# Optimization experiments

Hardware: AMD Instinct MI355X
Metric: run time of the kernel (lower is better)

The kernel has to match this reference:

```python
import jax, jax.numpy as jnp
import numpy as np

N_NODES = 100000
N_EDGES = 600000
HIDDEN = 128
LN_EPS = 1e-8


def setup_inputs() -> dict:
    key = jax.random.key(0)
    k1, k2, k3 = jax.random.split(key, 3)
    x = jax.random.normal(k1, (N_NODES, HIDDEN), dtype=jnp.float32)
    edge_index = jax.random.randint(k2, (2, N_EDGES), 0, N_NODES, dtype=jnp.int32)
    # GCNConv linear weight (glorot-ish scale) and bias
    W = jax.random.normal(k3, (HIDDEN, HIDDEN), dtype=jnp.float32) / np.sqrt(HIDDEN)
    b = jnp.zeros((HIDDEN,), dtype=jnp.float32)
    ln_gamma = jnp.ones((HIDDEN,), dtype=jnp.float32)
    ln_beta = jnp.zeros((HIDDEN,), dtype=jnp.float32)
    return {"x": x, "edge_index": edge_index, "W": W, "b": b,
            "ln_gamma": ln_gamma, "ln_beta": ln_beta}


def _gcn_layer(x, edge_index, W, b, ln_gamma, ln_beta):
    n = x.shape[0]
    # --- GCNConv (PyG semantics): add self-loops, sym-normalize, x@W, scatter ---
    loop = jnp.arange(n, dtype=edge_index.dtype)
    src = jnp.concatenate([edge_index[0], loop])  # [E+N]
    dst = jnp.concatenate([edge_index[1], loop])
    deg = jax.ops.segment_sum(jnp.ones_like(dst, dtype=x.dtype), dst,
                              num_segments=n)  # in-degree incl. self-loop
    dinv = jnp.where(deg > 0, jax.lax.rsqrt(deg), 0.0)
    norm = dinv[src] * dinv[dst]  # [E+N]
    h = x @ W  # [N, H]
    msg = h[src] * norm[:, None]  # gather + scale, [E+N, H]
    agg = jax.ops.segment_sum(msg, dst, num_segments=n) + b  # scatter-sum
    # --- ReLU -> (dropout = identity in eval) -> residual -> LayerNorm ---
    y = jax.nn.relu(agg) + x
    mu = jnp.mean(y, axis=-1, keepdims=True)
    var = jnp.mean(jnp.square(y - mu), axis=-1, keepdims=True)
    return (y - mu) * jax.lax.rsqrt(var + LN_EPS) * ln_gamma + ln_beta


def reference(x, edge_index, W, b, ln_gamma, ln_beta):
    return _gcn_layer(x, edge_index, W, b, ln_gamma, ln_beta)
```

## Files before the change

### kernel.cpp

```cpp
#include <hip/hip_runtime.h>

#define HID 128
#define CAP 32

typedef unsigned short u16;
typedef unsigned int u32;
typedef __attribute__((ext_vector_type(8))) short short8v;
typedef __attribute__((ext_vector_type(4))) float f32x4;
typedef __attribute__((ext_vector_type(4))) u32 u32x4;

__device__ inline u16 f2bf(float f) {
    union { float f; u32 u; } c; c.f = f;
    u32 u = c.u;
    return (u16)((u + 0x7FFFu + ((u >> 16) & 1u)) >> 16);
}
__device__ inline u32 pack2(float lo, float hi) {
    return (u32)f2bf(lo) | ((u32)f2bf(hi) << 16);
}
__device__ inline float bflo(u32 u) {
    union { u32 u; float f; } c; c.u = u << 16; return c.f;
}
__device__ inline float bfhi(u32 u) {
    union { u32 u; float f; } c; c.u = u & 0xFFFF0000u; return c.f;
}

__global__ void k_countfill(const int* __restrict__ src, const int* __restrict__ dst,
                            int* __restrict__ cnt, int* __restrict__ csr, int e) {
    int i = blockIdx.x * blockDim.x + threadIdx.x;
    if (i < e) {
        int d = dst[i];
        int slot = atomicAdd(&cnt[d], 1);
        if (slot < CAP) csr[(size_t)d * CAP + slot] = src[i];
    }
}

__global__ void k_prep(const int* __restrict__ cnt, float* __restrict__ dinv,
                       const float* __restrict__ W, u16* __restrict__ wswz, int n) {
    int t = blockIdx.x * blockDim.x + threadIdx.x;
    if (t < n) dinv[t] = rsqrtf((float)(cnt[t] + 1));
    if (t < 128 * 128) {
        int i = t & 7;
        int lane = (t >> 3) & 63;
        int ct = (t >> 9) & 7;
        int ks = t >> 12;
        int k = ks * 32 + (lane >> 4) * 8 + i;
        int col = ct * 16 + (lane & 15);
        wswz[t] = f2bf(W[k * HID + col]);
    }
}

__global__ __launch_bounds__(256) void k_gemm(const float* __restrict__ x,
                                              const u16* __restrict__ wswz,
                                              u16* __restrict__ hbf, int n) {
    __shared__ uint4 lds4[2048];
    char* lds = (char*)lds4;
    const int tid = threadIdx.x;
    const int row0 = blockIdx.x * 128;

    #pragma unroll
    for (int it = 0; it < 8; ++it) {
        int c = it * 256 + tid;
        int row = c >> 4;
        int c8 = (c & 15) * 8;
        uint4 payload;
        int gr = row0 + row;
        if (gr < n) {
            const float4* p = (const float4*)&x[(size_t)gr * HID + c8];
            float4 v0 = p[0], v1 = p[1];
            payload.x = pack2(v0.x, v0.y);
            payload.y = pack2(v0.z, v0.w);
            payload.z = pack2(v1.x, v1.y);
            payload.w = pack2(v1.z, v1.w);
        } else {
            payload = make_uint4(0, 0, 0, 0);
        }
        int byte = row * 256 + (c & 15) * 16;
        byte ^= (row & 7) << 4;
        *(uint4*)(lds + byte) = payload;
    }
    __syncthreads();

    const int w = tid >> 6;
    const int l = tid & 63;
    const short8v* wfrag = (const short8v*)wswz;

    f32x4 acc[2][8];
    #pragma unroll
    for (int r = 0; r < 2; ++r)
        #pragma unroll
        for (int c = 0; c < 8; ++c)
            acc[r][c] = (f32x4){0.f, 0.f, 0.f, 0.f};

    #pragma unroll
    for (int ks = 0; ks < 4; ++ks) {
        short8v a[2];
        #pragma unroll
        for (int rt = 0; rt < 2; ++rt) {
            int row = (w * 2 + rt) * 16 + (l & 15);
            int byte = row * 256 + ks * 64 + (l >> 4) * 16;
            byte ^= (row & 7) << 4;
            a[rt] = *(const short8v*)(lds + byte);
        }
        #pragma unroll
        for (int ct = 0; ct < 8; ++ct) {
            short8v b = wfrag[(ks * 8 + ct) * 64 + l];
            acc[0][ct] = __builtin_amdgcn_mfma_f32_16x16x32_bf16(a[0], b, acc[0][ct], 0, 0, 0);
            acc[1][ct] = __builtin_amdgcn_mfma_f32_16x16x32_bf16(a[1], b, acc[1][ct], 0, 0, 0);
        }
    }

    const bool even = ((l & 1) == 0);
    const int c15 = l & 15;
    #pragma unroll
    for (int rt = 0; rt < 2; ++rt) {
        #pragma unroll
        for (int j = 0; j < 4; ++j) {
            int gr = row0 + (w * 2 + rt) * 16 + (l >> 4) * 4 + j;
            char* rowp = (char*)(hbf + (size_t)gr * HID);
            #pragma unroll
            for (int p = 0; p < 4; ++p) {
                float a0 = acc[rt][2 * p][j];
                float a1 = acc[rt][2 * p + 1][j];
                float b0 = __shfl_xor(a0, 1);
                float b1 = __shfl_xor(a1, 1);
                float lo = even ? a0 : b1;
                float hi = even ? b0 : a1;
                u32 wd;
                asm("v_cvt_pk_bf16_f32 %0, %1, %2" : "=v"(wd) : "v"(lo), "v"(hi));
                int byte = p * 64 + (even ? c15 * 2 : 32 + (c15 - 1) * 2);
                if (gr < n) *(u32*)(rowp + byte) = wd;
            }
        }
    }
}

__global__ __launch_bounds__(256) void k_aggln(const float* __restrict__ x,
                                               const u16* __restrict__ hbf,
                                               const float* __restrict__ dinv,
                                               const int* __restrict__ cnt,
                                               const int* __restrict__ csr,
                                               const float* __restrict__ bvec,
                                               const float* __restrict__ gamma,
                                               const float* __restrict__ beta,
                                               float* __restrict__ out, int n) {
    int t = blockIdx.x * blockDim.x + threadIdx.x;
    int g = t >> 4;
    int l = t & 15;
    if (g >= n) return;
    const int j8 = l * 8;
    const float dd = dinv[g];

    float acc[8];
    {
        const float4* bp = (const float4*)&bvec[j8];
        float4 b0 = bp[0], b1 = bp[1];
        acc[0] = b0.x; acc[1] = b0.y; acc[2] = b0.z; acc[3] = b0.w;
        acc[4] = b1.x; acc[5] = b1.y; acc[6] = b1.z; acc[7] = b1.w;
    }
    {
        float s2 = dd * dd;
        u32x4 hv = *(const u32x4*)&hbf[(size_t)g * HID + j8];
        acc[0] = fmaf(bflo(hv.x), s2, acc[0]);
        acc[1] = fmaf(bfhi(hv.x), s2, acc[1]);
        acc[2] = fmaf(bflo(hv.y), s2, acc[2]);
        acc[3] = fmaf(bfhi(hv.y), s2, acc[3]);
        acc[4] = fmaf(bflo(hv.z), s2, acc[4]);
        acc[5] = fmaf(bfhi(hv.z), s2, acc[5]);
        acc[6] = fmaf(bflo(hv.w), s2, acc[6]);
        acc[7] = fmaf(bfhi(hv.w), s2, acc[7]);
    }

    const size_t off = (size_t)g * CAP;
    const int len = min(cnt[g], CAP);
    for (int base = 0; base < len; base += 16) {
        int idx = base + l;
        int sk = __builtin_nontemporal_load(&csr[off + (idx < len ? idx : 0)]);
        float dv = (idx < len) ? dinv[sk] : 0.f;
        int m4 = min(16, len - base);
        int mm = (m4 + 3) & ~3;
        for (int j = 0; j < mm; j += 4) {
            int s0 = __shfl(sk, j + 0, 16);
            int s1 = __shfl(sk, j + 1, 16);
            int s2 = __shfl(sk, j + 2, 16);
            int s3 = __shfl(sk, j + 3, 16);
            float w0 = __shfl(dv, j + 0, 16) * dd;
            float w1 = __shfl(dv, j + 1, 16) * dd;
            float w2 = __shfl(dv, j + 2, 16) * dd;
            float w3 = __shfl(dv, j + 3, 16) * dd;
            u32x4 h0 = *(const u32x4*)&hbf[(size_t)s0 * HID + j8];
            u32x4 h1 = *(const u32x4*)&hbf[(size_t)s1 * HID + j8];
            u32x4 h2 = *(const u32x4*)&hbf[(size_t)s2 * HID + j8];
            u32x4 h3 = *(const u32x4*)&hbf[(size_t)s3 * HID + j8];
            acc[0] = fmaf(bflo(h0.x), w0, acc[0]); acc[1] = fmaf(bfhi(h0.x), w0, acc[1]);
            acc[2] = fmaf(bflo(h0.y), w0, acc[2]); acc[3] = fmaf(bfhi(h0.y), w0, acc[3]);
            acc[4] = fmaf(bflo(h0.z), w0, acc[4]); acc[5] = fmaf(bfhi(h0.z), w0, acc[5]);
            acc[6] = fmaf(bflo(h0.w), w0, acc[6]); acc[7] = fmaf(bfhi(h0.w), w0, acc[7]);
            acc[0] = fmaf(bflo(h1.x), w1, acc[0]); acc[1] = fmaf(bfhi(h1.x), w1, acc[1]);
            acc[2] = fmaf(bflo(h1.y), w1, acc[2]); acc[3] = fmaf(bfhi(h1.y), w1, acc[3]);
            acc[4] = fmaf(bflo(h1.z), w1, acc[4]); acc[5] = fmaf(bfhi(h1.z), w1, acc[5]);
            acc[6] = fmaf(bflo(h1.w), w1, acc[6]); acc[7] = fmaf(bfhi(h1.w), w1, acc[7]);
            acc[0] = fmaf(bflo(h2.x), w2, acc[0]); acc[1] = fmaf(bfhi(h2.x), w2, acc[1]);
            acc[2] = fmaf(bflo(h2.y), w2, acc[2]); acc[3] = fmaf(bfhi(h2.y), w2, acc[3]);
            acc[4] = fmaf(bflo(h2.z), w2, acc[4]); acc[5] = fmaf(bfhi(h2.z), w2, acc[5]);
            acc[6] = fmaf(bflo(h2.w), w2, acc[6]); acc[7] = fmaf(bfhi(h2.w), w2, acc[7]);
            acc[0] = fmaf(bflo(h3.x), w3, acc[0]); acc[1] = fmaf(bfhi(h3.x), w3, acc[1]);
            acc[2] = fmaf(bflo(h3.y), w3, acc[2]); acc[3] = fmaf(bfhi(h3.y), w3, acc[3]);
            acc[4] = fmaf(bflo(h3.z), w3, acc[4]); acc[5] = fmaf(bfhi(h3.z), w3, acc[5]);
            acc[6] = fmaf(bflo(h3.w), w3, acc[6]); acc[7] = fmaf(bfhi(h3.w), w3, acc[7]);
        }
    }

    float y[8];
    {
        const f32x4* xp = (const f32x4*)&x[(size_t)g * HID + j8];
        f32x4 x0 = __builtin_nontemporal_load(xp);
        f32x4 x1 = __builtin_nontemporal_load(xp + 1);
        y[0] = fmaxf(acc[0], 0.f) + x0.x;
        y[1] = fmaxf(acc[1], 0.f) + x0.y;
        y[2] = fmaxf(acc[2], 0.f) + x0.z;
        y[3] = fmaxf(acc[3], 0.f) + x0.w;
        y[4] = fmaxf(acc[4], 0.f) + x1.x;
        y[5] = fmaxf(acc[5], 0.f) + x1.y;
        y[6] = fmaxf(acc[6], 0.f) + x1.z;
        y[7] = fmaxf(acc[7], 0.f) + x1.w;
    }

    float sum = 0.f;
    #pragma unroll
    for (int i = 0; i < 8; ++i) sum += y[i];
    #pragma unroll
    for (int o = 8; o > 0; o >>= 1) sum += __shfl_xor(sum, o);
    float mu = sum * (1.0f / HID);
    float vs = 0.f;
    float d[8];
    #pragma unroll
    for (int i = 0; i < 8; ++i) { d[i] = y[i] - mu; vs = fmaf(d[i], d[i], vs); }
    #pragma unroll
    for (int o = 8; o > 0; o >>= 1) vs += __shfl_xor(vs, o);
    float inv = rsqrtf(vs * (1.0f / HID) + 1e-8f);

    const float4* gp = (const float4*)&gamma[j8];
    const float4* bp = (const float4*)&beta[j8];
    float4 g0 = gp[0], g1 = gp[1];
    float4 be0 = bp[0], be1 = bp[1];
    f32x4 o0 = {fmaf(d[0] * inv, g0.x, be0.x), fmaf(d[1] * inv, g0.y, be0.y),
                fmaf(d[2] * inv, g0.z, be0.z), fmaf(d[3] * inv, g0.w, be0.w)};
    f32x4 o1 = {fmaf(d[4] * inv, g1.x, be1.x), fmaf(d[5] * inv, g1.y, be1.y),
                fmaf(d[6] * inv, g1.z, be1.z), fmaf(d[7] * inv, g1.w, be1.w)};
    f32x4* op = (f32x4*)&out[(size_t)g * HID + j8];
    __builtin_nontemporal_store(o0, op);
    __builtin_nontemporal_store(o1, op + 1);
}

extern "C" void kernel_launch(void* const* d_in, const int* in_sizes, int n_in,
                              void* d_out, int out_size, void* d_ws, size_t ws_size,
                              hipStream_t stream) {
    const float* x     = (const float*)d_in[0];
    const int*   ei    = (const int*)d_in[1];
    const float* W     = (const float*)d_in[2];
    const float* b     = (const float*)d_in[3];
    const float* gamma = (const float*)d_in[4];
    const float* beta  = (const float*)d_in[5];
    float* out = (float*)d_out;

    const int n = in_sizes[0] / HID;
    const int e = in_sizes[1] / 2;
    const int* src = ei;
    const int* dst = ei + e;

    u16* hbf    = (u16*)d_ws;
    int* cnt    = (int*)(hbf + (size_t)n * HID);
    float* dinv = (float*)(cnt + n);
    int* csr    = (int*)(dinv + n);
    u16* wswz   = (u16*)(csr + (size_t)n * CAP);

    hipMemsetAsync(cnt, 0, (size_t)n * sizeof(int), stream);
    k_countfill<<<(e + 255) / 256, 256, 0, stream>>>(src, dst, cnt, csr, e);
    k_prep<<<(n + 255) / 256, 256, 0, stream>>>(cnt, dinv, W, wswz, n);

    k_gemm<<<(n + 127) / 128, 256, 0, stream>>>(x, wswz, hbf, n);

    k_aggln<<<((size_t)n * 16 + 255) / 256, 256, 0, stream>>>(
        x, hbf, dinv, cnt, csr, b, gamma, beta, out, n);
}
```

Before: 112.2 us.

## Aggregate neighbors before the linear transform and fuse GEMM with LayerNorm epilogue

The GCN layer is reordered from A·(xW) to (A·x)·W. A bf16 copy of x is made in the prep kernel, neighbors are gathered and normalized into LDS tiles, and the tile is multiplied by W with MFMA. Bias, ReLU, residual and LayerNorm are applied in the GEMM epilogue, removing the separate aggregation kernel and the h intermediate. The trade-off is that each group of 16 threads now walks 8 rows one after another, which gives less latency hiding for the gathers. The epilogue also uses column-strided scalar loads and stores instead of vector accesses.

Result: slower. 119.1 us (+6.1%).

```diff
diff --git a/kernel.cpp b/kernel.cpp
--- a/kernel.cpp
+++ b/kernel.cpp
@@ -34,9 +34,24 @@
     }
 }
 
-__global__ void k_prep(const int* __restrict__ cnt, float* __restrict__ dinv,
-                       const float* __restrict__ W, u16* __restrict__ wswz, int n) {
+__global__ __launch_bounds__(256) void k_prep(const float* __restrict__ x,
+                                              u16* __restrict__ xbf,
+                                              const int* __restrict__ cnt,
+                                              float* __restrict__ dinv,
+                                              const float* __restrict__ W,
+                                              u16* __restrict__ wswz, int n) {
     int t = blockIdx.x * blockDim.x + threadIdx.x;
+    if (t < n * 16) {
+        int g = t >> 4, l = t & 15;
+        const float4* p = (const float4*)&x[(size_t)g * HID + l * 8];
+        float4 v0 = p[0], v1 = p[1];
+        uint4 o;
+        o.x = pack2(v0.x, v0.y);
+        o.y = pack2(v0.z, v0.w);
+        o.z = pack2(v1.x, v1.y);
+        o.w = pack2(v1.z, v1.w);
+        *(uint4*)&xbf[(size_t)g * HID + l * 8] = o;
+    }
     if (t < n) dinv[t] = rsqrtf((float)(cnt[t] + 1));
     if (t < 128 * 128) {
         int i = t & 7;
@@ -49,39 +64,93 @@
     }
 }
 
-__global__ __launch_bounds__(256) void k_gemm(const float* __restrict__ x,
-                                              const u16* __restrict__ wswz,
-                                              u16* __restrict__ hbf, int n) {
+__global__ __launch_bounds__(256) void k_fused(const float* __restrict__ x,
+                                               const u16* __restrict__ xbf,
+                                               const float* __restrict__ dinv,
+                                               const int* __restrict__ cnt,
+                                               const int* __restrict__ csr,
+                                               const u16* __restrict__ wswz,
+                                               const float* __restrict__ bvec,
+                                               const float* __restrict__ gamma,
+                                               const float* __restrict__ beta,
+                                               float* __restrict__ out, int n) {
     __shared__ uint4 lds4[2048];
     char* lds = (char*)lds4;
     const int tid = threadIdx.x;
     const int row0 = blockIdx.x * 128;
 
-    #pragma unroll
-    for (int it = 0; it < 8; ++it) {
-        int c = it * 256 + tid;
-        int row = c >> 4;
-        int c8 = (c & 15) * 8;
-        uint4 payload;
-        int gr = row0 + row;
-        if (gr < n) {
-            const float4* p = (const float4*)&x[(size_t)gr * HID + c8];
-            float4 v0 = p[0], v1 = p[1];
-            payload.x = pack2(v0.x, v0.y);
-            payload.y = pack2(v0.z, v0.w);
-            payload.z = pack2(v1.x, v1.y);
-            payload.w = pack2(v1.z, v1.w);
-        } else {
-            payload = make_uint4(0, 0, 0, 0);
-        }
-        int byte = row * 256 + (c & 15) * 16;
-        byte ^= (row & 7) << 4;
-        *(uint4*)(lds + byte) = payload;
+    {
+        const int grp = tid >> 4;
+        const int l16 = tid & 15;
+        const int j8 = l16 * 8;
+        for (int k = 0; k < 8; ++k) {
+            int r = grp * 8 + k;
+            int g = row0 + r;
+            uint4 pk = make_uint4(0, 0, 0, 0);
+            if (g < n) {
+                const float dd = dinv[g];
+                float acc[8];
+                {
+                    float s2 = dd * dd;
+                    u32x4 hv = *(const u32x4*)&xbf[(size_t)g * HID + j8];
+                    acc[0] = bflo(hv.x) * s2; acc[1] = bfhi(hv.x) * s2;
+                    acc[2] = bflo(hv.y) * s2; acc[3] = bfhi(hv.y) * s2;
+                    acc[4] = bflo(hv.z) * s2; acc[5] = bfhi(hv.z) * s2;
+                    acc[6] = bflo(hv.w) * s2; acc[7] = bfhi(hv.w) * s2;
+                }
+                const size_t off = (size_t)g * CAP;
+                const int len = min(cnt[g], CAP);
+                for (int base = 0; base < len; base += 16) {
+                    int idx = base + l16;
+                    int sk = csr[off + (idx < len ? idx : 0)];
+                    float dv = (idx < len) ? dinv[sk] : 0.f;
+                    int mm = (min(16, len - base) + 3) & ~3;
+                    for (int j = 0; j < mm; j += 4) {
+                        int s0 = __shfl(sk, j + 0, 16);
+                        int s1 = __shfl(sk, j + 1, 16);
+                        int s2 = __shfl(sk, j + 2, 16);
+                        int s3 = __shfl(sk, j + 3, 16);
+                        float w0 = __shfl(dv, j + 0, 16) * dd;
+                        float w1 = __shfl(dv, j + 1, 16) * dd;
+                        float w2 = __shfl(dv, j + 2, 16) * dd;
+                        float w3 = __shfl(dv, j + 3, 16) * dd;
+                        u32x4 h0 = *(const u32x4*)&xbf[(size_t)s0 * HID + j8];
+                        u32x4 h1 = *(const u32x4*)&xbf[(size_t)s1 * HID + j8];
+                        u32x4 h2 = *(const u32x4*)&xbf[(size_t)s2 * HID + j8];
+                        u32x4 h3 = *(const u32x4*)&xbf[(size_t)s3 * HID + j8];
+                        acc[0] = fmaf(bflo(h0.x), w0, acc[0]); acc[1] = fmaf(bfhi(h0.x), w0, acc[1]);
+                        acc[2] = fmaf(bflo(h0.y), w0, acc[2]); acc[3] = fmaf(bfhi(h0.y), w0, acc[3]);
+                        acc[4] = fmaf(bflo(h0.z), w0, acc[4]); acc[5] = fmaf(bfhi(h0.z), w0, acc[5]);
+                        acc[6] = fmaf(bflo(h0.w), w0, acc[6]); acc[7] = fmaf(bfhi(h0.w), w0, acc[7]);
+                        acc[0] = fmaf(bflo(h1.x), w1, acc[0]); acc[1] = fmaf(bfhi(h1.x), w1, acc[1]);
+                        acc[2] = fmaf(bflo(h1.y), w1, acc[2]); acc[3] = fmaf(bfhi(h1.y), w1, acc[3]);
+                        acc[4] = fmaf(bflo(h1.z), w1, acc[4]); acc[5] = fmaf(bfhi(h1.z), w1, acc[5]);
+                        acc[6] = fmaf(bflo(h1.w), w1, acc[6]); acc[7] = fmaf(bfhi(h1.w), w1, acc[7]);
+                        acc[0] = fmaf(bflo(h2.x), w2, acc[0]); acc[1] = fmaf(bfhi(h2.x), w2, acc[1]);
+                        acc[2] = fmaf(bflo(h2.y), w2, acc[2]); acc[3] = fmaf(bfhi(h2.y), w2, acc[3]);
+                        acc[4] = fmaf(bflo(h2.z), w2, acc[4]); acc[5] = fmaf(bfhi(h2.z), w2, acc[5]);
+                        acc[6] = fmaf(bflo(h2.w), w2, acc[6]); acc[7] = fmaf(bfhi(h2.w), w2, acc[7]);
+                        acc[0] = fmaf(bflo(h3.x), w3, acc[0]); acc[1] = fmaf(bfhi(h3.x), w3, acc[1]);
+                        acc[2] = fmaf(bflo(h3.y), w3, acc[2]); acc[3] = fmaf(bfhi(h3.y), w3, acc[3]);
+                        acc[4] = fmaf(bflo(h3.z), w3, acc[4]); acc[5] = fmaf(bfhi(h3.z), w3, acc[5]);
+                        acc[6] = fmaf(bflo(h3.w), w3, acc[6]); acc[7] = fmaf(bfhi(h3.w), w3, acc[7]);
+                    }
+                }
+                pk.x = pack2(acc[0], acc[1]);
+                pk.y = pack2(acc[2], acc[3]);
+                pk.z = pack2(acc[4], acc[5]);
+                pk.w = pack2(acc[6], acc[7]);
+            }
+            int byte = r * 256 + l16 * 16;
+            byte ^= (r & 7) << 4;
+            *(uint4*)(lds + byte) = pk;
+        }
     }
     __syncthreads();
 
     const int w = tid >> 6;
     const int l = tid & 63;
+    const int c15 = l & 15;
     const short8v* wfrag = (const short8v*)wswz;
 
     f32x4 acc[2][8];
@@ -96,7 +165,7 @@
         short8v a[2];
         #pragma unroll
         for (int rt = 0; rt < 2; ++rt) {
-            int row = (w * 2 + rt) * 16 + (l & 15);
+            int row = (w * 2 + rt) * 16 + c15;
             int byte = row * 256 + ks * 64 + (l >> 4) * 16;
             byte ^= (row & 7) << 4;
             a[rt] = *(const short8v*)(lds + byte);
@@ -109,147 +178,43 @@
         }
     }
 
-    const bool even = ((l & 1) == 0);
-    const int c15 = l & 15;
+    float bb[8], gg[8], bz[8];
+    #pragma unroll
+    for (int ct = 0; ct < 8; ++ct) {
+        bb[ct] = bvec[ct * 16 + c15];
+        gg[ct] = gamma[ct * 16 + c15];
+        bz[ct] = beta[ct * 16 + c15];
+    }
     #pragma unroll
     for (int rt = 0; rt < 2; ++rt) {
         #pragma unroll
         for (int j = 0; j < 4; ++j) {
             int gr = row0 + (w * 2 + rt) * 16 + (l >> 4) * 4 + j;
-            char* rowp = (char*)(hbf + (size_t)gr * HID);
-            #pragma unroll
-            for (int p = 0; p < 4; ++p) {
-                float a0 = acc[rt][2 * p][j];
-                float a1 = acc[rt][2 * p + 1][j];
-                float b0 = __shfl_xor(a0, 1);
-                float b1 = __shfl_xor(a1, 1);
-                float lo = even ? a0 : b1;
-                float hi = even ? b0 : a1;
-                u32 wd;
-                asm("v_cvt_pk_bf16_f32 %0, %1, %2" : "=v"(wd) : "v"(lo), "v"(hi));
-                int byte = p * 64 + (even ? c15 * 2 : 32 + (c15 - 1) * 2);
-                if (gr < n) *(u32*)(rowp + byte) = wd;
+            if (gr < n) {
+                const float* xr = x + (size_t)gr * HID + c15;
+                float v[8];
+                #pragma unroll
+                for (int ct = 0; ct < 8; ++ct)
+                    v[ct] = fmaxf(acc[rt][ct][j] + bb[ct], 0.f) + xr[ct * 16];
+                float sum = 0.f;
+                #pragma unroll
+                for (int ct = 0; ct < 8; ++ct) sum += v[ct];
+                #pragma unroll
+                for (int o = 1; o < 16; o <<= 1) sum += __shfl_xor(sum, o, 16);
+                float mu = sum * (1.0f / HID);
+                float d[8], vs = 0.f;
+                #pragma unroll
+                for (int ct = 0; ct < 8; ++ct) { d[ct] = v[ct] - mu; vs = fmaf(d[ct], d[ct], vs); }
+                #pragma unroll
+                for (int o = 1; o < 16; o <<= 1) vs += __shfl_xor(vs, o, 16);
+                float inv = rsqrtf(vs * (1.0f / HID) + 1e-8f);
+                float* orow = out + (size_t)gr * HID + c15;
+                #pragma unroll
+                for (int ct = 0; ct < 8; ++ct)
+                    __builtin_nontemporal_store(fmaf(d[ct] * inv, gg[ct], bz[ct]), &orow[ct * 16]);
             }
         }
     }
-}
-
-__global__ __launch_bounds__(256) void k_aggln(const float* __restrict__ x,
-                                               const u16* __restrict__ hbf,
-                                               const float* __restrict__ dinv,
-                                               const int* __restrict__ cnt,
-                                               const int* __restrict__ csr,
-                                               const float* __restrict__ bvec,
-                                               const float* __restrict__ gamma,
-                                               const float* __restrict__ beta,
-                                               float* __restrict__ out, int n) {
-    int t = blockIdx.x * blockDim.x + threadIdx.x;
-    int g = t >> 4;
-    int l = t & 15;
-    if (g >= n) return;
-    const int j8 = l * 8;
-    const float dd = dinv[g];
-
-    float acc[8];
-    {
-        const float4* bp = (const float4*)&bvec[j8];
-        float4 b0 = bp[0], b1 = bp[1];
-        acc[0] = b0.x; acc[1] = b0.y; acc[2] = b0.z; acc[3] = b0.w;
-        acc[4] = b1.x; acc[5] = b1.y; acc[6] = b1.z; acc[7] = b1.w;
-    }
-    {
-        float s2 = dd * dd;
-        u32x4 hv = *(const u32x4*)&hbf[(size_t)g * HID + j8];
-        acc[0] = fmaf(bflo(hv.x), s2, acc[0]);
-        acc[1] = fmaf(bfhi(hv.x), s2, acc[1]);
-        acc[2] = fmaf(bflo(hv.y), s2, acc[2]);
-        acc[3] = fmaf(bfhi(hv.y), s2, acc[3]);
-        acc[4] = fmaf(bflo(hv.z), s2, acc[4]);
-        acc[5] = fmaf(bfhi(hv.z), s2, acc[5]);
-        acc[6] = fmaf(bflo(hv.w), s2, acc[6]);
-        acc[7] = fmaf(bfhi(hv.w), s2, acc[7]);
-    }
-
-    const size_t off = (size_t)g * CAP;
-    const int len = min(cnt[g], CAP);
-    for (int base = 0; base < len; base += 16) {
-        int idx = base + l;
-        int sk = __builtin_nontemporal_load(&csr[off + (idx < len ? idx : 0)]);
-        float dv = (idx < len) ? dinv[sk] : 0.f;
-        int m4 = min(16, len - base);
-        int mm = (m4 + 3) & ~3;
-        for (int j = 0; j < mm; j += 4) {
-            int s0 = __shfl(sk, j + 0, 16);
-            int s1 = __shfl(sk, j + 1, 16);
-            int s2 = __shfl(sk, j + 2, 16);
-            int s3 = __shfl(sk, j + 3, 16);
-            float w0 = __shfl(dv, j + 0, 16) * dd;
-            float w1 = __shfl(dv, j + 1, 16) * dd;
-            float w2 = __shfl(dv, j + 2, 16) * dd;
-            float w3 = __shfl(dv, j + 3, 16) * dd;
-            u32x4 h0 = *(const u32x4*)&hbf[(size_t)s0 * HID + j8];
-            u32x4 h1 = *(const u32x4*)&hbf[(size_t)s1 * HID + j8];
-            u32x4 h2 = *(const u32x4*)&hbf[(size_t)s2 * HID + j8];
-            u32x4 h3 = *(const u32x4*)&hbf[(size_t)s3 * HID + j8];
-            acc[0] = fmaf(bflo(h0.x), w0, acc[0]); acc[1] = fmaf(bfhi(h0.x), w0, acc[1]);
-            acc[2] = fmaf(bflo(h0.y), w0, acc[2]); acc[3] = fmaf(bfhi(h0.y), w0, acc[3]);
-            acc[4] = fmaf(bflo(h0.z), w0, acc[4]); acc[5] = fmaf(bfhi(h0.z), w0, acc[5]);
-            acc[6] = fmaf(bflo(h0.w), w0, acc[6]); acc[7] = fmaf(bfhi(h0.w), w0, acc[7]);
-            acc[0] = fmaf(bflo(h1.x), w1, acc[0]); acc[1] = fmaf(bfhi(h1.x), w1, acc[1]);
-            acc[2] = fmaf(bflo(h1.y), w1, acc[2]); acc[3] = fmaf(bfhi(h1.y), w1, acc[3]);
-            acc[4] = fmaf(bflo(h1.z), w1, acc[4]); acc[5] = fmaf(bfhi(h1.z), w1, acc[5]);
-            acc[6] = fmaf(bflo(h1.w), w1, acc[6]); acc[7] = fmaf(bfhi(h1.w), w1, acc[7]);
-            acc[0] = fmaf(bflo(h2.x), w2, acc[0]); acc[1] = fmaf(bfhi(h2.x), w2, acc[1]);
-            acc[2] = fmaf(bflo(h2.y), w2, acc[2]); acc[3] = fmaf(bfhi(h2.y), w2, acc[3]);
-            acc[4] = fmaf(bflo(h2.z), w2, acc[4]); acc[5] = fmaf(bfhi(h2.z), w2, acc[5]);
-            acc[6] = fmaf(bflo(h2.w), w2, acc[6]); acc[7] = fmaf(bfhi(h2.w), w2, acc[7]);
-            acc[0] = fmaf(bflo(h3.x), w3, acc[0]); acc[1] = fmaf(bfhi(h3.x), w3, acc[1]);
-            acc[2] = fmaf(bflo(h3.y), w3, acc[2]); acc[3] = fmaf(bfhi(h3.y), w3, acc[3]);
-            acc[4] = fmaf(bflo(h3.z), w3, acc[4]); acc[5] = fmaf(bfhi(h3.z), w3, acc[5]);
-            acc[6] = fmaf(bflo(h3.w), w3, acc[6]); acc[7] = fmaf(bfhi(h3.w), w3, acc[7]);
-        }
-    }
-
-    float y[8];
-    {
-        const f32x4* xp = (const f32x4*)&x[(size_t)g * HID + j8];
-        f32x4 x0 = __builtin_nontemporal_load(xp);
-        f32x4 x1 = __builtin_nontemporal_load(xp + 1);
-        y[0] = fmaxf(acc[0], 0.f) + x0.x;
-        y[1] = fmaxf(acc[1], 0.f) + x0.y;
-        y[2] = fmaxf(acc[2], 0.f) + x0.z;
-        y[3] = fmaxf(acc[3], 0.f) + x0.w;
-        y[4] = fmaxf(acc[4], 0.f) + x1.x;
-        y[5] = fmaxf(acc[5], 0.f) + x1.y;
-        y[6] = fmaxf(acc[6], 0.f) + x1.z;
-        y[7] = fmaxf(acc[7], 0.f) + x1.w;
-    }
-
-    float sum = 0.f;
-    #pragma unroll
-    for (int i = 0; i < 8; ++i) sum += y[i];
-    #pragma unroll
-    for (int o = 8; o > 0; o >>= 1) sum += __shfl_xor(sum, o);
-    float mu = sum * (1.0f / HID);
-    float vs = 0.f;
-    float d[8];
-    #pragma unroll
-    for (int i = 0; i < 8; ++i) { d[i] = y[i] - mu; vs = fmaf(d[i], d[i], vs); }
-    #pragma unroll
-    for (int o = 8; o > 0; o >>= 1) vs += __shfl_xor(vs, o);
-    float inv = rsqrtf(vs * (1.0f / HID) + 1e-8f);
-
-    const float4* gp = (const float4*)&gamma[j8];
-    const float4* bp = (const float4*)&beta[j8];
-    float4 g0 = gp[0], g1 = gp[1];
-    float4 be0 = bp[0], be1 = bp[1];
-    f32x4 o0 = {fmaf(d[0] * inv, g0.x, be0.x), fmaf(d[1] * inv, g0.y, be0.y),
-                fmaf(d[2] * inv, g0.z, be0.z), fmaf(d[3] * inv, g0.w, be0.w)};
-    f32x4 o1 = {fmaf(d[4] * inv, g1.x, be1.x), fmaf(d[5] * inv, g1.y, be1.y),
-                fmaf(d[6] * inv, g1.z, be1.z), fmaf(d[7] * inv, g1.w, be1.w)};
-    f32x4* op = (f32x4*)&out[(size_t)g * HID + j8];
-    __builtin_nontemporal_store(o0, op);
-    __builtin_nontemporal_store(o1, op + 1);
 }
 
 extern "C" void kernel_launch(void* const* d_in, const int* in_sizes, int n_in,
@@ -268,18 +233,16 @@
     const int* src = ei;
     const int* dst = ei + e;
 
-    u16* hbf    = (u16*)d_ws;
-    int* cnt    = (int*)(hbf + (size_t)n * HID);
+    u16* xbf    = (u16*)d_ws;
+    int* cnt    = (int*)(xbf + (size_t)n * HID);
     float* dinv = (float*)(cnt + n);
     int* csr    = (int*)(dinv + n);
     u16* wswz   = (u16*)(csr + (size_t)n * CAP);
 
     hipMemsetAsync(cnt, 0, (size_t)n * sizeof(int), stream);
     k_countfill<<<(e + 255) / 256, 256, 0, stream>>>(src, dst, cnt, csr, e);
-    k_prep<<<(n + 255) / 256, 256, 0, stream>>>(cnt, dinv, W, wswz, n);
-
-    k_gemm<<<(n + 127) / 128, 256, 0, stream>>>(x, wswz, hbf, n);
-
-    k_aggln<<<((size_t)n * 16 + 255) / 256, 256, 0, stream>>>(
-        x, hbf, dinv, cnt, csr, b, gamma, beta, out, n);
-}
+    k_prep<<<((size_t)n * 16 + 255) / 256, 256, 0, stream>>>(x, xbf, cnt, dinv, W, wswz, n);
+
+    k_fused<<<(n + 127) / 128, 256, 0, stream>>>(
+        x, xbf, dinv, cnt, csr, wswz, b, gamma, beta, out, n);
+}
```
